# Optimization experiments

Measured on AMD Instinct MI355X. Metric: run time of the kernel, lower is better.

The kernel has to match this reference:

```python
import jax, jax.numpy as jnp
import numpy as np

K = 1024
D = 64
BETA = 0.25
EPS = 1e-10


def setup_inputs() -> dict:
    key = jax.random.key(0)
    k1, k2 = jax.random.split(key)
    z = jax.random.normal(k1, (64, D, 32, 32), dtype=jnp.float32)
    # embedding.weight.data.uniform_(-1/K, 1/K)
    emb = jax.random.uniform(k2, (K, D), dtype=jnp.float32,
                             minval=-1.0 / K, maxval=1.0 / K)
    return {"z": z, "emb": emb}


def reference(z, emb):
    sg = jax.lax.stop_gradient
    B, C, H, W = z.shape  # C == D
    zp = jnp.transpose(z, (0, 2, 3, 1))            # [B,H,W,D]
    zf = zp.reshape(-1, C)                          # [N,D]
    # squared-euclidean distances via matmul (cdist expansion)
    d = (jnp.sum(zf ** 2, axis=1, keepdims=True)
         + jnp.sum(emb ** 2, axis=1)
         - 2.0 * jnp.matmul(zf, emb.T))             # [N,K]
    idx = jnp.argmin(d, axis=1)                     # [N] int
    z_q = emb[idx].reshape(zp.shape)                # gather == one-hot matmul
    loss = (jnp.mean((sg(z_q) - zp) ** 2)
            + BETA * jnp.mean((z_q - sg(zp)) ** 2))
    # straight-through estimator
    z_q_st = zp + sg(z_q - zp)
    # codebook usage perplexity
    n = zf.shape[0]
    e_mean = jnp.zeros((K,), dtype=zf.dtype).at[idx].add(1.0) / n
    perplexity = jnp.exp(-jnp.sum(e_mean * jnp.log(e_mean + EPS)))
    z_q_out = jnp.transpose(z_q_st, (0, 3, 1, 2))   # back to [B,D,H,W]
    return (loss, z_q_out, perplexity, idx.reshape(B, H, W))
```

## Files before the change

kernel.cpp:

```cpp
#include <hip/hip_runtime.h>

#define NVEC 65536
#define KC   1024
#define DD   64
#define NTILE 64
#define KTILE 128
#define ETS  136

#define OUT_ZQ   1
#define OUT_PPL  4194305
#define OUT_IDX  4194306

#define WS_KEYS  0
#define WS_HIST  524288
#define WS_SUMSQ 528384
#define WS_SE    528392

__global__ __launch_bounds__(256) void prep_emb(const float* __restrict__ emb,
                                                float* __restrict__ se) {
    const int k = blockIdx.x * 256 + threadIdx.x;
    const float* er = emb + (size_t)k * 64;
    float r[8];
    #pragma unroll
    for (int c = 0; c < 64; ++c) {
        float v = er[c];
        float s = __fmul_rn(v, v);
        if (c < 8) r[c] = s;
        else       r[c & 7] = __fadd_rn(r[c & 7], s);
    }
    se[k] = __fadd_rn(__fadd_rn(__fadd_rn(r[0], r[1]), __fadd_rn(r[2], r[3])),
                      __fadd_rn(__fadd_rn(r[4], r[5]), __fadd_rn(r[6], r[7])));
}

__global__ __launch_bounds__(256)
void dist_kernel(const float* __restrict__ z,
                 const float* __restrict__ emb,
                 const float* __restrict__ se,
                 unsigned long long* __restrict__ keys) {
    __shared__ float zt[64][64];
    __shared__ float et[64][ETS];
    __shared__ float lds_sz[64];
    __shared__ unsigned long long red[64];

    const int tid = threadIdx.x;
    const int tn  = tid & 15;
    const int tk  = tid >> 4;
    const int n0  = blockIdx.x * NTILE;
    const int b   = n0 >> 10;
    const int hw0 = n0 & 1023;

    {
        const float* zbase = z + (size_t)b * 65536 + hw0;
        #pragma unroll
        for (int j = 0; j < 4; ++j) {
            int idx = tid + j * 256;
            int c   = idx >> 4;
            int nl4 = (idx & 15) * 4;
            float4 v = *(const float4*)(zbase + (size_t)c * 1024 + nl4);
            *(float4*)&zt[c][nl4] = v;
        }
        if (tid < 64) red[tid] = 0xFFFFFFFFFFFFFFFFULL;
    }
    __syncthreads();

    if (tid < 64) {
        float r[8];
        #pragma unroll
        for (int c = 0; c < 64; ++c) {
            float v = zt[c][tid];
            float s = __fmul_rn(v, v);
            if (c < 8) r[c] = s;
            else       r[c & 7] = __fadd_rn(r[c & 7], s);
        }
        lds_sz[tid] = __fadd_rn(
            __fadd_rn(__fadd_rn(r[0], r[1]), __fadd_rn(r[2], r[3])),
            __fadd_rn(__fadd_rn(r[4], r[5]), __fadd_rn(r[6], r[7])));
    }

    float dbest[4] = {3.4e38f, 3.4e38f, 3.4e38f, 3.4e38f};
    int   kbest[4] = {0, 0, 0, 0};

    for (int t = 0; t < KC / KTILE; ++t) {
        const int k0 = t * KTILE;

        {
            int k  = tid >> 1;
            int cq = tid & 1;
            const float* erow = emb + (size_t)(k0 + k) * 64;
            #pragma unroll
            for (int q = 0; q < 8; ++q) {
                int cb = cq * 4 + q * 8;
                float4 v = *(const float4*)(erow + cb);
                et[cb + 0][k] = v.x;
                et[cb + 1][k] = v.y;
                et[cb + 2][k] = v.z;
                et[cb + 3][k] = v.w;
            }
        }
        __syncthreads();

        float acc[4][8];
        #pragma unroll
        for (int i = 0; i < 4; ++i)
            #pragma unroll
            for (int j = 0; j < 8; ++j) acc[i][j] = 0.0f;

        #pragma unroll 4
        for (int c = 0; c < 64; ++c) {
            const float4 zv  = *(const float4*)&zt[c][tn * 4];
            const float4 ev0 = *(const float4*)&et[c][tk * 8];
            const float4 ev1 = *(const float4*)&et[c][tk * 8 + 4];
            const float zr[4] = {zv.x, zv.y, zv.z, zv.w};
            const float er[8] = {ev0.x, ev0.y, ev0.z, ev0.w,
                                 ev1.x, ev1.y, ev1.z, ev1.w};
            #pragma unroll
            for (int i = 0; i < 4; ++i)
                #pragma unroll
                for (int j = 0; j < 8; ++j)
                    acc[i][j] = __fmaf_rn(zr[i], er[j], acc[i][j]);
        }

        const float4 sev0 = *(const float4*)(se + k0 + tk * 8);
        const float4 sev1 = *(const float4*)(se + k0 + tk * 8 + 4);
        const float ses[8] = {sev0.x, sev0.y, sev0.z, sev0.w,
                              sev1.x, sev1.y, sev1.z, sev1.w};
        const float4 szv = *(const float4*)&lds_sz[tn * 4];
        const float szs[4] = {szv.x, szv.y, szv.z, szv.w};

        #pragma unroll
        for (int i = 0; i < 4; ++i)
            #pragma unroll
            for (int j = 0; j < 8; ++j) {
                float d = __fsub_rn(__fadd_rn(szs[i], ses[j]),
                                    __fmul_rn(2.0f, acc[i][j]));
                if (d < dbest[i]) { dbest[i] = d; kbest[i] = k0 + tk * 8 + j; }
            }
        __syncthreads();
    }

    #pragma unroll
    for (int i = 0; i < 4; ++i) {
        unsigned m = __float_as_uint(dbest[i]);
        m ^= ((int)m < 0) ? 0xFFFFFFFFu : 0x80000000u;
        atomicMin(&red[tn * 4 + i],
                  ((unsigned long long)m << 10) | (unsigned)kbest[i]);
    }
    __syncthreads();
    if (tid < 64) keys[n0 + tid] = red[tid];
}

__global__ __launch_bounds__(256) void epilogue_kernel(const float* __restrict__ z,
                                                       const float* __restrict__ emb,
                                                       const unsigned long long* __restrict__ keys,
                                                       float* __restrict__ out,
                                                       int* __restrict__ hist,
                                                       double* __restrict__ sumsq) {
    __shared__ double red[256];
    const int tid = threadIdx.x;
    const int n   = blockIdx.x * 256 + tid;
    const int b   = n >> 10;
    const int hw  = n & 1023;
    const int idx = (int)(keys[n] & 1023ULL);

    out[OUT_IDX + n] = (float)idx;
    atomicAdd(&hist[idx], 1);

    const float* zp = z   + (size_t)b * 65536 + hw;
    float*       op = out + OUT_ZQ + (size_t)b * 65536 + hw;
    const float* er = emb + (size_t)idx * DD;
    double s = 0.0;
    #pragma unroll
    for (int c = 0; c < DD; ++c) {
        float zv   = zp[(size_t)c * 1024];
        float ev   = er[c];
        float diff = ev - zv;
        op[(size_t)c * 1024] = zv + diff;
        s = fma((double)diff, (double)diff, s);
    }
    red[tid] = s;
    __syncthreads();
    for (int off = 128; off > 0; off >>= 1) {
        if (tid < off) red[tid] += red[tid + off];
        __syncthreads();
    }
    if (tid == 0) atomicAdd(sumsq, red[0]);
}

__global__ __launch_bounds__(256) void final_kernel(const int* __restrict__ hist,
                                                    const double* __restrict__ sumsq,
                                                    float* __restrict__ out) {
    __shared__ double red[256];
    const int tid = threadIdx.x;
    double s = 0.0;
    #pragma unroll
    for (int j = 0; j < 4; ++j) {
        int   kk = j * 256 + tid;
        float em = (float)hist[kk] * (1.0f / 65536.0f);
        float t  = em * logf(em + 1e-10f);
        s += (double)t;
    }
    red[tid] = s;
    __syncthreads();
    for (int off = 128; off > 0; off >>= 1) {
        if (tid < off) red[tid] += red[tid + off];
        __syncthreads();
    }
    if (tid == 0) {
        out[OUT_PPL] = expf(-(float)red[0]);
        out[0]       = 1.25f * (float)(sumsq[0] / 4194304.0);
    }
}

extern "C" void kernel_launch(void* const* d_in, const int* in_sizes, int n_in,
                              void* d_out, int out_size, void* d_ws, size_t ws_size,
                              hipStream_t stream) {
    const float* z   = (const float*)d_in[0];
    const float* emb = (const float*)d_in[1];
    float* out = (float*)d_out;
    char*  ws  = (char*)d_ws;

    unsigned long long* keys  = (unsigned long long*)(ws + WS_KEYS);
    int*                hist  = (int*)(ws + WS_HIST);
    double*             sumsq = (double*)(ws + WS_SUMSQ);
    float*              se    = (float*)(ws + WS_SE);

    hipMemsetAsync(hist, 0, (size_t)KC * 4 + 8, stream);

    prep_emb<<<KC / 256, 256, 0, stream>>>(emb, se);
    dist_kernel<<<NVEC / NTILE, 256, 0, stream>>>(z, emb, se, keys);
    epilogue_kernel<<<NVEC / 256, 256, 0, stream>>>(z, emb, keys, out, hist, sumsq);
    final_kernel<<<1, 256, 0, stream>>>(hist, sumsq, out);
}
```

Before: 146.3 us.

## Fuse epilogue into distance kernel and prefetch codebook tiles into registers

Merges the epilogue into the distance kernel. Each block reuses its z tile already held in LDS to write z_q, the index output and the histogram entries, and to accumulate the squared error with a wavefront shuffle reduction. This removes a launch, the keys round trip through global memory and a second read of z. The codebook tile for the next iteration is prefetched into registers to overlap the global loads with compute. It also removes the LDS padding on et, raises the inner unroll, uses an fma for the distance, and sets waves_per_eu(3), which may add LDS bank conflicts and register pressure.

```diff
diff --git a/kernel.cpp b/kernel.cpp
--- a/kernel.cpp
+++ b/kernel.cpp
@@ -5,16 +5,14 @@
 #define DD   64
 #define NTILE 64
 #define KTILE 128
-#define ETS  136
 
 #define OUT_ZQ   1
 #define OUT_PPL  4194305
 #define OUT_IDX  4194306
 
-#define WS_KEYS  0
-#define WS_HIST  524288
-#define WS_SUMSQ 528384
-#define WS_SE    528392
+#define WS_HIST  0
+#define WS_SUMSQ 4096
+#define WS_SE    4104
 
 __global__ __launch_bounds__(256) void prep_emb(const float* __restrict__ emb,
                                                 float* __restrict__ se) {
@@ -33,12 +31,15 @@
 }
 
 __global__ __launch_bounds__(256)
-void dist_kernel(const float* __restrict__ z,
-                 const float* __restrict__ emb,
-                 const float* __restrict__ se,
-                 unsigned long long* __restrict__ keys) {
+__attribute__((amdgpu_waves_per_eu(3)))
+void dist_fused(const float* __restrict__ z,
+                const float* __restrict__ emb,
+                const float* __restrict__ se,
+                float* __restrict__ out,
+                int* __restrict__ hist,
+                double* __restrict__ sumsq) {
     __shared__ float zt[64][64];
-    __shared__ float et[64][ETS];
+    __shared__ float et[64][KTILE];
     __shared__ float lds_sz[64];
     __shared__ unsigned long long red[64];
 
@@ -56,10 +57,18 @@
             int idx = tid + j * 256;
             int c   = idx >> 4;
             int nl4 = (idx & 15) * 4;
-            float4 v = *(const float4*)(zbase + (size_t)c * 1024 + nl4);
-            *(float4*)&zt[c][nl4] = v;
+            *(float4*)&zt[c][nl4] = *(const float4*)(zbase + (size_t)c * 1024 + nl4);
         }
         if (tid < 64) red[tid] = 0xFFFFFFFFFFFFFFFFULL;
+    }
+
+    const int krow = tid >> 1;
+    const int cq   = tid & 1;
+    float4 pf[8];
+    {
+        const float* er = emb + (size_t)krow * 64 + cq * 4;
+        #pragma unroll
+        for (int q = 0; q < 8; ++q) pf[q] = *(const float4*)(er + q * 8);
     }
     __syncthreads();
 
@@ -81,21 +90,18 @@
     int   kbest[4] = {0, 0, 0, 0};
 
     for (int t = 0; t < KC / KTILE; ++t) {
-        const int k0 = t * KTILE;
-
-        {
-            int k  = tid >> 1;
-            int cq = tid & 1;
-            const float* erow = emb + (size_t)(k0 + k) * 64;
-            #pragma unroll
-            for (int q = 0; q < 8; ++q) {
-                int cb = cq * 4 + q * 8;
-                float4 v = *(const float4*)(erow + cb);
-                et[cb + 0][k] = v.x;
-                et[cb + 1][k] = v.y;
-                et[cb + 2][k] = v.z;
-                et[cb + 3][k] = v.w;
-            }
+        #pragma unroll
+        for (int q = 0; q < 8; ++q) {
+            int cb = cq * 4 + q * 8;
+            et[cb + 0][krow] = pf[q].x;
+            et[cb + 1][krow] = pf[q].y;
+            et[cb + 2][krow] = pf[q].z;
+            et[cb + 3][krow] = pf[q].w;
+        }
+        if (t + 1 < KC / KTILE) {
+            const float* er = emb + (size_t)((t + 1) * KTILE + krow) * 64 + cq * 4;
+            #pragma unroll
+            for (int q = 0; q < 8; ++q) pf[q] = *(const float4*)(er + q * 8);
         }
         __syncthreads();
 
@@ -105,7 +111,7 @@
             #pragma unroll
             for (int j = 0; j < 8; ++j) acc[i][j] = 0.0f;
 
-        #pragma unroll 4
+        #pragma unroll 8
         for (int c = 0; c < 64; ++c) {
             const float4 zv  = *(const float4*)&zt[c][tn * 4];
             const float4 ev0 = *(const float4*)&et[c][tk * 8];
@@ -120,6 +126,7 @@
                     acc[i][j] = __fmaf_rn(zr[i], er[j], acc[i][j]);
         }
 
+        const int k0 = t * KTILE;
         const float4 sev0 = *(const float4*)(se + k0 + tk * 8);
         const float4 sev1 = *(const float4*)(se + k0 + tk * 8 + 4);
         const float ses[8] = {sev0.x, sev0.y, sev0.z, sev0.w,
@@ -131,8 +138,8 @@
         for (int i = 0; i < 4; ++i)
             #pragma unroll
             for (int j = 0; j < 8; ++j) {
-                float d = __fsub_rn(__fadd_rn(szs[i], ses[j]),
-                                    __fmul_rn(2.0f, acc[i][j]));
+                float s = __fadd_rn(szs[i], ses[j]);
+                float d = __fmaf_rn(-2.0f, acc[i][j], s);
                 if (d < dbest[i]) { dbest[i] = d; kbest[i] = k0 + tk * 8 + j; }
             }
         __syncthreads();
@@ -146,44 +153,29 @@
                   ((unsigned long long)m << 10) | (unsigned)kbest[i]);
     }
     __syncthreads();
-    if (tid < 64) keys[n0 + tid] = red[tid];
-}
-
-__global__ __launch_bounds__(256) void epilogue_kernel(const float* __restrict__ z,
-                                                       const float* __restrict__ emb,
-                                                       const unsigned long long* __restrict__ keys,
-                                                       float* __restrict__ out,
-                                                       int* __restrict__ hist,
-                                                       double* __restrict__ sumsq) {
-    __shared__ double red[256];
-    const int tid = threadIdx.x;
-    const int n   = blockIdx.x * 256 + tid;
-    const int b   = n >> 10;
-    const int hw  = n & 1023;
-    const int idx = (int)(keys[n] & 1023ULL);
-
-    out[OUT_IDX + n] = (float)idx;
-    atomicAdd(&hist[idx], 1);
-
-    const float* zp = z   + (size_t)b * 65536 + hw;
-    float*       op = out + OUT_ZQ + (size_t)b * 65536 + hw;
-    const float* er = emb + (size_t)idx * DD;
+
+    const int nl   = tid & 63;
+    const int idxn = (int)(red[nl] & 1023ULL);
+    if (tid < 64) {
+        out[OUT_IDX + n0 + tid] = (float)idxn;
+        atomicAdd(&hist[idxn], 1);
+    }
+    const float* erow  = emb + (size_t)idxn * 64;
+    float*       obase = out + OUT_ZQ + (size_t)b * 65536 + hw0 + nl;
+    const int c0 = tid >> 6;
     double s = 0.0;
     #pragma unroll
-    for (int c = 0; c < DD; ++c) {
-        float zv   = zp[(size_t)c * 1024];
-        float ev   = er[c];
+    for (int j = 0; j < 16; ++j) {
+        int   c    = c0 + j * 4;
+        float zv   = zt[c][nl];
+        float ev   = erow[c];
         float diff = ev - zv;
-        op[(size_t)c * 1024] = zv + diff;
+        obase[(size_t)c * 1024] = zv + diff;
         s = fma((double)diff, (double)diff, s);
     }
-    red[tid] = s;
-    __syncthreads();
-    for (int off = 128; off > 0; off >>= 1) {
-        if (tid < off) red[tid] += red[tid + off];
-        __syncthreads();
-    }
-    if (tid == 0) atomicAdd(sumsq, red[0]);
+    #pragma unroll
+    for (int off = 32; off; off >>= 1) s += __shfl_down(s, off, 64);
+    if ((tid & 63) == 0) atomicAdd(sumsq, s);
 }
 
 __global__ __launch_bounds__(256) void final_kernel(const int* __restrict__ hist,
@@ -219,15 +211,13 @@
     float* out = (float*)d_out;
     char*  ws  = (char*)d_ws;
 
-    unsigned long long* keys  = (unsigned long long*)(ws + WS_KEYS);
-    int*                hist  = (int*)(ws + WS_HIST);
-    double*             sumsq = (double*)(ws + WS_SUMSQ);
-    float*              se    = (float*)(ws + WS_SE);
+    int*    hist  = (int*)(ws + WS_HIST);
+    double* sumsq = (double*)(ws + WS_SUMSQ);
+    float*  se    = (float*)(ws + WS_SE);
 
     hipMemsetAsync(hist, 0, (size_t)KC * 4 + 8, stream);
 
     prep_emb<<<KC / 256, 256, 0, stream>>>(emb, se);
-    dist_kernel<<<NVEC / NTILE, 256, 0, stream>>>(z, emb, se, keys);
-    epilogue_kernel<<<NVEC / 256, 256, 0, stream>>>(z, emb, keys, out, hist, sumsq);
+    dist_fused<<<NVEC / NTILE, 256, 0, stream>>>(z, emb, se, out, hist, sumsq);
     final_kernel<<<1, 256, 0, stream>>>(hist, sumsq, out);
 }
```

New measurement: 152.0 us. 3.9% more time.

## Pre-transpose codebook and stream it via wave-uniform scalar loads in distance kernel

Applied to the files above, without the earlier changes.

A prep kernel now writes a transposed copy of the codebook alongside the norms. The distance kernel drops the per-tile LDS staging of the codebook: each wave takes a 256-entry slice of codes, and each lane owns one vector. Codebook values are read with wave-uniform addresses (likely scalar loads) and broadcast into 32-wide accumulator groups. This removes LDS traffic and most block barriers, but relies on scalar cache bandwidth and latency, and folds the distance combine into an fma that changes rounding slightly.

```diff
diff --git a/kernel.cpp b/kernel.cpp
--- a/kernel.cpp
+++ b/kernel.cpp
@@ -4,8 +4,8 @@
 #define KC   1024
 #define DD   64
 #define NTILE 64
-#define KTILE 128
-#define ETS  136
+#define KW   256
+#define KU   32
 
 #define OUT_ZQ   1
 #define OUT_PPL  4194305
@@ -15,39 +15,66 @@
 #define WS_HIST  524288
 #define WS_SUMSQ 528384
 #define WS_SE    528392
-
-__global__ __launch_bounds__(256) void prep_emb(const float* __restrict__ emb,
-                                                float* __restrict__ se) {
-    const int k = blockIdx.x * 256 + threadIdx.x;
-    const float* er = emb + (size_t)k * 64;
-    float r[8];
+#define WS_EMBT  532488
+
+__global__ __launch_bounds__(256) void prep_kernel(const float* __restrict__ emb,
+                                                   float* __restrict__ se,
+                                                   float* __restrict__ embT) {
+    __shared__ float tile[64][65];
+    const int tid = threadIdx.x;
+    const int k0  = blockIdx.x * 64;
+
+    {
+        const int r = tid >> 2, q = tid & 3;
+        const float* row = emb + (size_t)(k0 + r) * 64 + q * 16;
+        #pragma unroll
+        for (int i = 0; i < 4; ++i) {
+            float4 v = *(const float4*)(row + i * 4);
+            tile[r][q * 16 + i * 4 + 0] = v.x;
+            tile[r][q * 16 + i * 4 + 1] = v.y;
+            tile[r][q * 16 + i * 4 + 2] = v.z;
+            tile[r][q * 16 + i * 4 + 3] = v.w;
+        }
+    }
+    __syncthreads();
+
+    if (tid < 64) {
+        float r[8];
+        #pragma unroll
+        for (int c = 0; c < 64; ++c) {
+            float v = tile[tid][c];
+            float s = __fmul_rn(v, v);
+            if (c < 8) r[c] = s;
+            else       r[c & 7] = __fadd_rn(r[c & 7], s);
+        }
+        se[k0 + tid] = __fadd_rn(
+            __fadd_rn(__fadd_rn(r[0], r[1]), __fadd_rn(r[2], r[3])),
+            __fadd_rn(__fadd_rn(r[4], r[5]), __fadd_rn(r[6], r[7])));
+    }
+
+    const int kl = tid & 63, cg = tid >> 6;
     #pragma unroll
-    for (int c = 0; c < 64; ++c) {
-        float v = er[c];
-        float s = __fmul_rn(v, v);
-        if (c < 8) r[c] = s;
-        else       r[c & 7] = __fadd_rn(r[c & 7], s);
-    }
-    se[k] = __fadd_rn(__fadd_rn(__fadd_rn(r[0], r[1]), __fadd_rn(r[2], r[3])),
-                      __fadd_rn(__fadd_rn(r[4], r[5]), __fadd_rn(r[6], r[7])));
+    for (int i = 0; i < 16; ++i) {
+        int c = cg * 16 + i;
+        embT[(size_t)c * KC + k0 + kl] = tile[kl][c];
+    }
 }
 
 __global__ __launch_bounds__(256)
 void dist_kernel(const float* __restrict__ z,
-                 const float* __restrict__ emb,
+                 const float* __restrict__ embT,
                  const float* __restrict__ se,
                  unsigned long long* __restrict__ keys) {
     __shared__ float zt[64][64];
-    __shared__ float et[64][ETS];
     __shared__ float lds_sz[64];
     __shared__ unsigned long long red[64];
 
-    const int tid = threadIdx.x;
-    const int tn  = tid & 15;
-    const int tk  = tid >> 4;
-    const int n0  = blockIdx.x * NTILE;
-    const int b   = n0 >> 10;
-    const int hw0 = n0 & 1023;
+    const int tid  = threadIdx.x;
+    const int lane = tid & 63;
+    const int w    = tid >> 6;
+    const int n0   = blockIdx.x * NTILE;
+    const int b    = n0 >> 10;
+    const int hw0  = n0 & 1023;
 
     {
         const float* zbase = z + (size_t)b * 65536 + hw0;
@@ -56,8 +83,7 @@
             int idx = tid + j * 256;
             int c   = idx >> 4;
             int nl4 = (idx & 15) * 4;
-            float4 v = *(const float4*)(zbase + (size_t)c * 1024 + nl4);
-            *(float4*)&zt[c][nl4] = v;
+            *(float4*)&zt[c][nl4] = *(const float4*)(zbase + (size_t)c * 1024 + nl4);
         }
         if (tid < 64) red[tid] = 0xFFFFFFFFFFFFFFFFULL;
     }
@@ -76,75 +102,40 @@
             __fadd_rn(__fadd_rn(r[0], r[1]), __fadd_rn(r[2], r[3])),
             __fadd_rn(__fadd_rn(r[4], r[5]), __fadd_rn(r[6], r[7])));
     }
-
-    float dbest[4] = {3.4e38f, 3.4e38f, 3.4e38f, 3.4e38f};
-    int   kbest[4] = {0, 0, 0, 0};
-
-    for (int t = 0; t < KC / KTILE; ++t) {
-        const int k0 = t * KTILE;
-
-        {
-            int k  = tid >> 1;
-            int cq = tid & 1;
-            const float* erow = emb + (size_t)(k0 + k) * 64;
+    __syncthreads();
+
+    const float szn = lds_sz[lane];
+    const int   kb  = __builtin_amdgcn_readfirstlane(w * KW);
+
+    float dbest = 3.4e38f;
+    int   kbestv = 0;
+
+    for (int g = 0; g < KW; g += KU) {
+        const int kg = kb + g;
+        float acc[KU];
+        #pragma unroll
+        for (int j = 0; j < KU; ++j) acc[j] = 0.0f;
+
+        #pragma unroll 2
+        for (int c = 0; c < 64; ++c) {
+            const float zc = zt[c][lane];
+            const float* __restrict__ eb = embT + (size_t)c * KC + kg;
             #pragma unroll
-            for (int q = 0; q < 8; ++q) {
-                int cb = cq * 4 + q * 8;
-                float4 v = *(const float4*)(erow + cb);
-                et[cb + 0][k] = v.x;
-                et[cb + 1][k] = v.y;
-                et[cb + 2][k] = v.z;
-                et[cb + 3][k] = v.w;
-            }
-        }
-        __syncthreads();
-
-        float acc[4][8];
-        #pragma unroll
-        for (int i = 0; i < 4; ++i)
-            #pragma unroll
-            for (int j = 0; j < 8; ++j) acc[i][j] = 0.0f;
-
-        #pragma unroll 4
-        for (int c = 0; c < 64; ++c) {
-            const float4 zv  = *(const float4*)&zt[c][tn * 4];
-            const float4 ev0 = *(const float4*)&et[c][tk * 8];
-            const float4 ev1 = *(const float4*)&et[c][tk * 8 + 4];
-            const float zr[4] = {zv.x, zv.y, zv.z, zv.w};
-            const float er[8] = {ev0.x, ev0.y, ev0.z, ev0.w,
-                                 ev1.x, ev1.y, ev1.z, ev1.w};
-            #pragma unroll
-            for (int i = 0; i < 4; ++i)
-                #pragma unroll
-                for (int j = 0; j < 8; ++j)
-                    acc[i][j] = __fmaf_rn(zr[i], er[j], acc[i][j]);
-        }
-
-        const float4 sev0 = *(const float4*)(se + k0 + tk * 8);
-        const float4 sev1 = *(const float4*)(se + k0 + tk * 8 + 4);
-        const float ses[8] = {sev0.x, sev0.y, sev0.z, sev0.w,
-                              sev1.x, sev1.y, sev1.z, sev1.w};
-        const float4 szv = *(const float4*)&lds_sz[tn * 4];
-        const float szs[4] = {szv.x, szv.y, szv.z, szv.w};
-
-        #pragma unroll
-        for (int i = 0; i < 4; ++i)
-            #pragma unroll
-            for (int j = 0; j < 8; ++j) {
-                float d = __fsub_rn(__fadd_rn(szs[i], ses[j]),
-                                    __fmul_rn(2.0f, acc[i][j]));
-                if (d < dbest[i]) { dbest[i] = d; kbest[i] = k0 + tk * 8 + j; }
-            }
-        __syncthreads();
-    }
-
-    #pragma unroll
-    for (int i = 0; i < 4; ++i) {
-        unsigned m = __float_as_uint(dbest[i]);
-        m ^= ((int)m < 0) ? 0xFFFFFFFFu : 0x80000000u;
-        atomicMin(&red[tn * 4 + i],
-                  ((unsigned long long)m << 10) | (unsigned)kbest[i]);
-    }
+            for (int j = 0; j < KU; ++j)
+                acc[j] = __fmaf_rn(zc, eb[j], acc[j]);
+        }
+
+        const float* __restrict__ sb = se + kg;
+        #pragma unroll
+        for (int j = 0; j < KU; ++j) {
+            float d = __fmaf_rn(-2.0f, acc[j], __fadd_rn(szn, sb[j]));
+            if (d < dbest) { dbest = d; kbestv = kg + j; }
+        }
+    }
+
+    unsigned m = __float_as_uint(dbest);
+    m ^= ((int)m < 0) ? 0xFFFFFFFFu : 0x80000000u;
+    atomicMin(&red[lane], ((unsigned long long)m << 10) | (unsigned)kbestv);
     __syncthreads();
     if (tid < 64) keys[n0 + tid] = red[tid];
 }
@@ -223,11 +214,12 @@
     int*                hist  = (int*)(ws + WS_HIST);
     double*             sumsq = (double*)(ws + WS_SUMSQ);
     float*              se    = (float*)(ws + WS_SE);
+    float*              embT  = (float*)(ws + WS_EMBT);
 
     hipMemsetAsync(hist, 0, (size_t)KC * 4 + 8, stream);
 
-    prep_emb<<<KC / 256, 256, 0, stream>>>(emb, se);
-    dist_kernel<<<NVEC / NTILE, 256, 0, stream>>>(z, emb, se, keys);
+    prep_kernel<<<KC / 64, 256, 0, stream>>>(emb, se, embT);
+    dist_kernel<<<NVEC / NTILE, 256, 0, stream>>>(z, embT, se, keys);
     epilogue_kernel<<<NVEC / 256, 256, 0, stream>>>(z, emb, keys, out, hist, sumsq);
     final_kernel<<<1, 256, 0, stream>>>(hist, sumsq, out);
 }
```

Measured after the change: 151.7 us. 3.7% more time.
